# Kernel tuning notes

Measured on AMD Instinct MI355X. Metric: run time of the kernel, lower is better.

The kernel has to match this reference:

```python
import jax, jax.numpy as jnp
import numpy as np

B, L, D, H = 4, 1024, 1024, 16
DH = D // H


def setup_inputs() -> dict:
    key = jax.random.key(0)
    ks = jax.random.split(key, 10)
    x_embed = jax.random.normal(ks[0], (B, L, D), dtype=jnp.float32)
    bemb = jax.random.normal(ks[1], (B, L), dtype=jnp.float32)
    s = 0.02
    Wq_w = jax.random.normal(ks[2], (D, D), dtype=jnp.float32) * s
    Wk_w = jax.random.normal(ks[3], (D, D), dtype=jnp.float32) * s
    Wv_w = jax.random.normal(ks[4], (D, D), dtype=jnp.float32) * s
    Wo_w = jax.random.normal(ks[5], (D, D), dtype=jnp.float32) * s
    Wq_b = jnp.zeros((D,), jnp.float32)
    Wk_b = jnp.zeros((D,), jnp.float32)
    Wv_b = jnp.zeros((D,), jnp.float32)
    Wo_b = jnp.zeros((D,), jnp.float32)
    return dict(x_embed=x_embed, bemb=bemb, Wq_w=Wq_w, Wq_b=Wq_b,
                Wk_w=Wk_w, Wk_b=Wk_b, Wv_w=Wv_w, Wv_b=Wv_b,
                Wo_w=Wo_w, Wo_b=Wo_b)


def reference(x_embed, bemb, Wq_w, Wq_b, Wk_w, Wk_b, Wv_w, Wv_b, Wo_w, Wo_b):
    # present[b, l] = token l of batch b participates in attention
    present = bemb > 0  # [B, L]

    def proj(w, b):
        # torch Linear: y = x W^T + b; split heads -> [B, H, L, DH]
        y = jnp.einsum('bld,ed->ble', x_embed, w) + b
        return y.reshape(B, L, H, DH).transpose(0, 2, 1, 3)

    Q = proj(Wq_w, Wq_b)
    K = proj(Wk_w, Wk_b)
    V = proj(Wv_w, Wv_b)

    scores = jnp.einsum('bhqd,bhkd->bhqk', Q, K) / jnp.sqrt(jnp.float32(DH))
    # pre-softmax column mask: absent keys -> -inf
    scores = jnp.where(present[:, None, None, :], scores, -jnp.inf)
    A = jax.nn.softmax(scores, axis=-1)  # [B, H, L, L]
    # post-softmax row mask: subtract 1 on absent query rows, then relu
    row_absent = (~present).astype(A.dtype)[:, None, :, None]  # [B,1,L,1]
    A = jnp.maximum(A - row_absent, 0.0)

    out = jnp.einsum('bhqk,bhkd->bhqd', A, V)
    out = out.transpose(0, 2, 1, 3).reshape(B, L, D)
    out = jnp.einsum('bld,ed->ble', out, Wo_w) + Wo_b
    return out, A
```

## Files before the change

### kernel.cpp

```cpp
#include <hip/hip_runtime.h>
#include <math.h>

#define BB 4
#define LL 1024
#define DD 1024
#define HH 16
#define MROWS 4096

typedef __attribute__((ext_vector_type(8))) short short8;
typedef __attribute__((ext_vector_type(4))) float f32x4;
typedef __attribute__((ext_vector_type(4))) unsigned short us4;

__device__ inline unsigned short f2bf(float f) {
    unsigned int u = __builtin_bit_cast(unsigned int, f);
    u += 0x7fffu + ((u >> 16) & 1u);
    return (unsigned short)(u >> 16);
}

__device__ inline void gl2lds16(const void* g, void* l) {
    __builtin_amdgcn_global_load_lds(
        (const __attribute__((address_space(1))) void*)g,
        (__attribute__((address_space(3))) void*)l, 16, 0, 0);
}

__global__ __launch_bounds__(256) void cvt_all(const float* __restrict__ x,
                                               const float* __restrict__ wq,
                                               const float* __restrict__ wk,
                                               const float* __restrict__ wv,
                                               const float* __restrict__ wo,
                                               unsigned short* __restrict__ xb,
                                               unsigned short* __restrict__ wqb,
                                               unsigned short* __restrict__ wkb,
                                               unsigned short* __restrict__ wvb,
                                               unsigned short* __restrict__ wob) {
    int i = blockIdx.x * 256 + threadIdx.x;
    const float* src; unsigned short* dst; int k;
    if (i < 1048576) { src = x; dst = xb; k = i; }
    else {
        int j = i - 1048576; int w = j >> 18; k = j & 262143;
        src = (w == 0) ? wq : (w == 1) ? wk : (w == 2) ? wv : wo;
        dst = (w == 0) ? wqb : (w == 1) ? wkb : (w == 2) ? wvb : wob;
    }
    float4 v = ((const float4*)src)[k];
    us4 p = { f2bf(v.x), f2bf(v.y), f2bf(v.z), f2bf(v.w) };
    ((us4*)dst)[k] = p;
}

template<int BM>
__device__ __forceinline__ void gemm_core(const unsigned short* __restrict__ X,
                                          const unsigned short* __restrict__ W,
                                          const float* __restrict__ bias,
                                          void* __restrict__ Cv, int out_mode) {
    constexpr int MI = BM / 32;
    __shared__ unsigned short SMEM[(BM + 128) * 64];
    auto Xs = (unsigned short(*)[64])SMEM;
    auto Ws = (unsigned short(*)[64])(SMEM + BM * 64);
    const int t = threadIdx.x;
    const int lane = t & 63, quad = lane >> 4, lm = lane & 15;
    const int wave = t >> 6;
    const int mo = (wave & 1) * (BM / 2), no = (wave >> 1) * 64;
    const int row0 = blockIdx.x * BM, col0 = blockIdx.y * 128;
    const int sw = lm & 7;

    const int r_in = lane >> 3;
    const int sg = (lane & 7) ^ r_in;
    const unsigned short* xp = X + (size_t)(row0 + wave * (BM / 4) + r_in) * 1024 + sg * 8;
    const unsigned short* wp = W + (size_t)(col0 + wave * 32 + r_in) * 1024 + sg * 8;
    unsigned short* ldsX = &Xs[wave * (BM / 4)][0];
    unsigned short* ldsW = &Ws[wave * 32][0];

    f32x4 acc[MI][4] = {};

    for (int kc = 0; kc < 1024; kc += 64) {
        #pragma unroll
        for (int j = 0; j < BM / 32; ++j)
            gl2lds16(xp + (size_t)j * 8192 + kc, ldsX + j * 512);
        #pragma unroll
        for (int j = 0; j < 4; ++j)
            gl2lds16(wp + (size_t)j * 8192 + kc, ldsW + j * 512);
        __syncthreads();
        #pragma unroll
        for (int s = 0; s < 2; ++s) {
            short8 af[MI], bf[4];
            #pragma unroll
            for (int mi = 0; mi < MI; ++mi)
                af[mi] = *(const short8*)&Xs[mo + mi * 16 + lm][((s * 4 + quad) ^ sw) * 8];
            #pragma unroll
            for (int nj = 0; nj < 4; ++nj)
                bf[nj] = *(const short8*)&Ws[no + nj * 16 + lm][((s * 4 + quad) ^ sw) * 8];
            #pragma unroll
            for (int mi = 0; mi < MI; ++mi)
                #pragma unroll
                for (int nj = 0; nj < 4; ++nj)
                    acc[mi][nj] = __builtin_amdgcn_mfma_f32_16x16x32_bf16(
                        af[mi], bf[nj], acc[mi][nj], 0, 0, 0);
        }
        __syncthreads();
    }

    if constexpr (BM == 128) {
        if (out_mode == 2) {
            unsigned short* Ct = &SMEM[0];
            #pragma unroll
            for (int mi = 0; mi < 4; ++mi) {
                #pragma unroll
                for (int nj = 0; nj < 4; ++nj) {
                    int ccol = no + nj * 16 + lm;
                    int crow0 = mo + mi * 16 + quad * 4;
                    float bv = bias[col0 + ccol];
                    us4 pk = { f2bf(acc[mi][nj][0] + bv), f2bf(acc[mi][nj][1] + bv),
                               f2bf(acc[mi][nj][2] + bv), f2bf(acc[mi][nj][3] + bv) };
                    *(us4*)&Ct[ccol * 128 + (crow0 ^ ((ccol & 15) << 3))] = pk;
                }
            }
            __syncthreads();
            const int b = row0 >> 10, l0c = row0 & 1023;
            #pragma unroll
            for (int it = 0; it < 8; ++it) {
                int cc = (t >> 4) + it * 16;
                int lb = (t & 15) * 8;
                short8 v = *(const short8*)&Ct[cc * 128 + (lb ^ ((cc & 15) << 3))];
                int gcol = col0 + cc;
                int hh = gcol >> 6, dd = gcol & 63;
                *(short8*)&((unsigned short*)Cv)[(((size_t)b * 16 + hh) * 64 + dd) * 1024 + l0c + lb] = v;
            }
            return;
        }
    }

    #pragma unroll
    for (int mi = 0; mi < MI; ++mi) {
        #pragma unroll
        for (int nj = 0; nj < 4; ++nj) {
            int gr0 = row0 + mo + mi * 16 + quad * 4;
            int gc  = col0 + no + nj * 16 + lm;
            float bv = bias[gc];
            #pragma unroll
            for (int r = 0; r < 4; ++r) {
                float val = acc[mi][nj][r] + bv;
                int gr = gr0 + r;
                if (out_mode == 0) {
                    ((float*)Cv)[(size_t)gr * 1024 + gc] = val;
                } else {
                    ((unsigned short*)Cv)[(size_t)gr * 1024 + gc] = f2bf(val);
                }
            }
        }
    }
}

__global__ __launch_bounds__(256) void qkv_proj(const unsigned short* __restrict__ xb,
                                                const unsigned short* __restrict__ wq,
                                                const unsigned short* __restrict__ wk,
                                                const unsigned short* __restrict__ wv,
                                                const float* __restrict__ bq,
                                                const float* __restrict__ bk,
                                                const float* __restrict__ bv,
                                                unsigned short* __restrict__ Qw,
                                                unsigned short* __restrict__ Kw,
                                                unsigned short* __restrict__ Vt) {
    const int z = blockIdx.z;
    const unsigned short* W = (z == 0) ? wq : (z == 1) ? wk : wv;
    const float* b = (z == 0) ? bq : (z == 1) ? bk : bv;
    void* C = (z == 0) ? (void*)Qw : (z == 1) ? (void*)Kw : (void*)Vt;
    gemm_core<128>(xb, W, b, C, (z == 2) ? 2 : 1);
}

__global__ __launch_bounds__(256) void out_proj(const unsigned short* __restrict__ Aw,
                                                const unsigned short* __restrict__ wo,
                                                const float* __restrict__ bo,
                                                float* __restrict__ out) {
    gemm_core<64>(Aw, wo, bo, out, 0);
}

__global__ __launch_bounds__(512) void attn_fused(const unsigned short* __restrict__ Qw,
                                                  const unsigned short* __restrict__ Kw,
                                                  const unsigned short* __restrict__ Vt,
                                                  const float* __restrict__ bemb,
                                                  float* __restrict__ Aout,
                                                  unsigned short* __restrict__ attn) {
    __shared__ unsigned short Ks[128][64];
    __shared__ unsigned short Vs[64][128];
    __shared__ unsigned short Ps[8][16][66];
    __shared__ float maskadd[1024];
    const int t = threadIdx.x;
    const int lane = t & 63, quad = lane >> 4, lm = lane & 15;
    const int w = t >> 6;
    const int bh = blockIdx.x;
    const int q0 = blockIdx.y * 128;
    const int b = bh >> 4, h = bh & 15;
    const int qrow_frag = q0 + w * 16 + lm;
    const int qrow_acc0 = q0 + w * 16 + quad * 4;
    const int swk = lm & 7;

    const int kr_in = lane >> 3;
    const int ksg = (lane & 7) ^ kr_in;
    const unsigned short* kp = Kw + (size_t)(b * 1024 + w * 16 + kr_in) * 1024 + h * 64 + ksg * 8;
    unsigned short* ldsK = &Ks[w * 16][0];
    const int vr_in = lane >> 4, vcg = lane & 15;
    const int vrow = w * 8 + vr_in;
    const unsigned short* vpbase = Vt + (size_t)bh * 64 * 1024;
    unsigned short* ldsV = &Vs[w * 8][0];

    for (int i = t; i < 1024; i += 512)
        maskadd[i] = (bemb[b * 1024 + i] > 0.f) ? 0.f : -1e30f;

    short8 afq[2];
    #pragma unroll
    for (int s = 0; s < 2; ++s)
        afq[s] = *(const short8*)&Qw[(size_t)(b * 1024 + qrow_frag) * 1024 +
                                     h * 64 + s * 32 + quad * 8];

    float lsum[4] = { 0.f, 0.f, 0.f, 0.f };

    __syncthreads();

    for (int c = 0; c < 8; ++c) {
        #pragma unroll
        for (int j = 0; j < 2; ++j)
            gl2lds16(kp + (size_t)(c * 128 + j * 8) * 1024, ldsK + j * 512);
        __syncthreads();

        f32x4 acc[8] = {};
        #pragma unroll
        for (int s = 0; s < 2; ++s)
            #pragma unroll
            for (int nj = 0; nj < 8; ++nj) {
                short8 bfk = *(const short8*)&Ks[nj * 16 + lm][((s * 4 + quad) ^ swk) * 8];
                acc[nj] = __builtin_amdgcn_mfma_f32_16x16x32_bf16(afq[s], bfk, acc[nj], 0, 0, 0);
            }

        #pragma unroll
        for (int nj = 0; nj < 8; ++nj) {
            float ma = maskadd[c * 128 + nj * 16 + lm];
            #pragma unroll
            for (int r = 0; r < 4; ++r)
                lsum[r] += __expf(acc[nj][r] * 0.125f + ma);
        }
        __syncthreads();
    }

    float fnorm[4];
    #pragma unroll
    for (int r = 0; r < 4; ++r) {
        float s = lsum[r];
        #pragma unroll
        for (int off = 8; off >= 1; off >>= 1)
            s += __shfl_xor(s, off, 64);
        bool qp = bemb[b * 1024 + qrow_acc0 + r] > 0.f;
        fnorm[r] = (qp && s > 0.f) ? (1.f / s) : 0.f;
    }

    f32x4 oacc[4] = {};
    for (int c = 0; c < 8; ++c) {
        #pragma unroll
        for (int j = 0; j < 2; ++j) {
            gl2lds16(kp + (size_t)(c * 128 + j * 8) * 1024, ldsK + j * 512);
            int rl = vrow + j * 4;
            int vsg = vcg ^ (rl & 15);
            gl2lds16(vpbase + (size_t)rl * 1024 + c * 128 + vsg * 8, ldsV + j * 512);
        }
        __syncthreads();

        f32x4 acc[8] = {};
        #pragma unroll
        for (int s = 0; s < 2; ++s)
            #pragma unroll
            for (int nj = 0; nj < 8; ++nj) {
                short8 bfk = *(const short8*)&Ks[nj * 16 + lm][((s * 4 + quad) ^ swk) * 8];
                acc[nj] = __builtin_amdgcn_mfma_f32_16x16x32_bf16(afq[s], bfk, acc[nj], 0, 0, 0);
            }

        #pragma unroll
        for (int half = 0; half < 2; ++half) {
            #pragma unroll
            for (int nj4 = 0; nj4 < 4; ++nj4) {
                int nj = half * 4 + nj4;
                float ma = maskadd[c * 128 + nj * 16 + lm];
                #pragma unroll
                for (int r = 0; r < 4; ++r) {
                    float p  = __expf(acc[nj][r] * 0.125f + ma);
                    float a  = p * fnorm[r];
                    Aout[((size_t)bh * 1024 + qrow_acc0 + r) * 1024 + c * 128 + nj * 16 + lm] = a;
                    Ps[w][quad * 4 + r][nj4 * 16 + lm] = f2bf(a);
                }
            }
            #pragma unroll
            for (int ks2 = 0; ks2 < 2; ++ks2) {
                int ks = half * 2 + ks2;
                short8 afp = *(const short8*)&Ps[w][lm][ks2 * 32 + quad * 8];
                #pragma unroll
                for (int nd = 0; nd < 4; ++nd) {
                    short8 bfv = *(const short8*)&Vs[nd * 16 + lm][((ks * 4 + quad) ^ lm) * 8];
                    oacc[nd] = __builtin_amdgcn_mfma_f32_16x16x32_bf16(afp, bfv, oacc[nd], 0, 0, 0);
                }
            }
        }
        __syncthreads();
    }

    #pragma unroll
    for (int nd = 0; nd < 4; ++nd)
        #pragma unroll
        for (int r = 0; r < 4; ++r)
            attn[(size_t)(b * 1024 + qrow_acc0 + r) * 1024 + h * 64 + nd * 16 + lm] =
                f2bf(oacc[nd][r]);
}

extern "C" void kernel_launch(void* const* d_in, const int* in_sizes, int n_in,
                              void* d_out, int out_size, void* d_ws, size_t ws_size,
                              hipStream_t stream) {
    const float* x    = (const float*)d_in[0];
    const float* bemb = (const float*)d_in[1];
    const float* Wq   = (const float*)d_in[2];
    const float* Wq_b = (const float*)d_in[3];
    const float* Wk   = (const float*)d_in[4];
    const float* Wk_b = (const float*)d_in[5];
    const float* Wv   = (const float*)d_in[6];
    const float* Wv_b = (const float*)d_in[7];
    const float* Wo   = (const float*)d_in[8];
    const float* Wo_b = (const float*)d_in[9];

    float* out  = (float*)d_out;
    float* Aout = out + (size_t)BB * LL * DD;

    unsigned short* x_bf  = (unsigned short*)d_ws;
    unsigned short* Wq_bf = x_bf  + (size_t)MROWS * DD;
    unsigned short* Wk_bf = Wq_bf + (size_t)DD * DD;
    unsigned short* Wv_bf = Wk_bf + (size_t)DD * DD;
    unsigned short* Wo_bf = Wv_bf + (size_t)DD * DD;
    unsigned short* Qw    = Wo_bf + (size_t)DD * DD;
    unsigned short* Kw    = Qw + (size_t)MROWS * DD;
    unsigned short* Vt    = Kw + (size_t)MROWS * DD;
    unsigned short* Aw    = x_bf;

    cvt_all<<<dim3(8192), dim3(256), 0, stream>>>(x, Wq, Wk, Wv, Wo,
                                                  x_bf, Wq_bf, Wk_bf, Wv_bf, Wo_bf);

    qkv_proj<<<dim3(MROWS / 128, DD / 128, 3), dim3(256), 0, stream>>>(
        x_bf, Wq_bf, Wk_bf, Wv_bf, Wq_b, Wk_b, Wv_b, Qw, Kw, Vt);

    attn_fused<<<dim3(BB * HH, LL / 128), dim3(512), 0, stream>>>(
        Qw, Kw, Vt, bemb, Aout, Aw);

    out_proj<<<dim3(MROWS / 64, DD / 128), dim3(256), 0, stream>>>(
        Aw, Wo_bf, Wo_b, out);
}
```

Baseline: 415.8 us.

## Split attention softmax-denominator pass into separate higher-parallelism kernel

Moves the first pass that computes softmax row sums out of the fused attention kernel into its own kernel. The new kernel uses 64-row query tiles with 256 threads, giving more blocks, and writes the row sums to a global workspace. The second kernel reads those sums and performs normalisation, the A output and the PV product. This is meant to improve GPU occupancy for the sum pass. It adds a launch and a global round trip for the sums, and the QK^T work is still computed twice.

```diff
diff --git a/kernel.cpp b/kernel.cpp
--- a/kernel.cpp
+++ b/kernel.cpp
@@ -173,10 +173,81 @@
     gemm_core<64>(Aw, wo, bo, out, 0);
 }
 
-__global__ __launch_bounds__(512) void attn_fused(const unsigned short* __restrict__ Qw,
+__global__ __launch_bounds__(256) void attn_pass1(const unsigned short* __restrict__ Qw,
+                                                  const unsigned short* __restrict__ Kw,
+                                                  const float* __restrict__ bemb,
+                                                  float* __restrict__ Ls) {
+    __shared__ unsigned short Ks[128][64];
+    __shared__ float maskadd[1024];
+    const int t = threadIdx.x;
+    const int lane = t & 63, quad = lane >> 4, lm = lane & 15;
+    const int w = t >> 6;
+    const int bh = blockIdx.x;
+    const int q0 = blockIdx.y * 64;
+    const int b = bh >> 4, h = bh & 15;
+    const int qrow_frag = q0 + w * 16 + lm;
+    const int qrow_acc0 = q0 + w * 16 + quad * 4;
+    const int swk = lm & 7;
+
+    const int kr_in = lane >> 3;
+    const int ksg = (lane & 7) ^ kr_in;
+    const unsigned short* kp = Kw + (size_t)(b * 1024 + w * 32 + kr_in) * 1024 + h * 64 + ksg * 8;
+    unsigned short* ldsK = &Ks[w * 32][0];
+
+    for (int i = t; i < 1024; i += 256)
+        maskadd[i] = (bemb[b * 1024 + i] > 0.f) ? 0.f : -1e30f;
+
+    short8 afq[2];
+    #pragma unroll
+    for (int s = 0; s < 2; ++s)
+        afq[s] = *(const short8*)&Qw[(size_t)(b * 1024 + qrow_frag) * 1024 +
+                                     h * 64 + s * 32 + quad * 8];
+
+    float lsum[4] = { 0.f, 0.f, 0.f, 0.f };
+
+    __syncthreads();
+
+    for (int c = 0; c < 8; ++c) {
+        #pragma unroll
+        for (int j = 0; j < 4; ++j)
+            gl2lds16(kp + (size_t)(c * 128 + j * 8) * 1024, ldsK + j * 512);
+        __syncthreads();
+
+        f32x4 acc[8] = {};
+        #pragma unroll
+        for (int s = 0; s < 2; ++s)
+            #pragma unroll
+            for (int nj = 0; nj < 8; ++nj) {
+                short8 bfk = *(const short8*)&Ks[nj * 16 + lm][((s * 4 + quad) ^ swk) * 8];
+                acc[nj] = __builtin_amdgcn_mfma_f32_16x16x32_bf16(afq[s], bfk, acc[nj], 0, 0, 0);
+            }
+
+        #pragma unroll
+        for (int nj = 0; nj < 8; ++nj) {
+            float ma = maskadd[c * 128 + nj * 16 + lm];
+            #pragma unroll
+            for (int r = 0; r < 4; ++r)
+                lsum[r] += __expf(acc[nj][r] * 0.125f + ma);
+        }
+        __syncthreads();
+    }
+
+    #pragma unroll
+    for (int r = 0; r < 4; ++r) {
+        float s = lsum[r];
+        #pragma unroll
+        for (int off = 8; off >= 1; off >>= 1)
+            s += __shfl_xor(s, off, 64);
+        if (lm == r)
+            Ls[(size_t)bh * 1024 + qrow_acc0 + r] = s;
+    }
+}
+
+__global__ __launch_bounds__(512) void attn_pass2(const unsigned short* __restrict__ Qw,
                                                   const unsigned short* __restrict__ Kw,
                                                   const unsigned short* __restrict__ Vt,
                                                   const float* __restrict__ bemb,
+                                                  const float* __restrict__ Ls,
                                                   float* __restrict__ Aout,
                                                   unsigned short* __restrict__ attn) {
     __shared__ unsigned short Ks[128][64];
@@ -211,45 +282,15 @@
         afq[s] = *(const short8*)&Qw[(size_t)(b * 1024 + qrow_frag) * 1024 +
                                      h * 64 + s * 32 + quad * 8];
 
-    float lsum[4] = { 0.f, 0.f, 0.f, 0.f };
-
-    __syncthreads();
-
-    for (int c = 0; c < 8; ++c) {
-        #pragma unroll
-        for (int j = 0; j < 2; ++j)
-            gl2lds16(kp + (size_t)(c * 128 + j * 8) * 1024, ldsK + j * 512);
-        __syncthreads();
-
-        f32x4 acc[8] = {};
-        #pragma unroll
-        for (int s = 0; s < 2; ++s)
-            #pragma unroll
-            for (int nj = 0; nj < 8; ++nj) {
-                short8 bfk = *(const short8*)&Ks[nj * 16 + lm][((s * 4 + quad) ^ swk) * 8];
-                acc[nj] = __builtin_amdgcn_mfma_f32_16x16x32_bf16(afq[s], bfk, acc[nj], 0, 0, 0);
-            }
-
-        #pragma unroll
-        for (int nj = 0; nj < 8; ++nj) {
-            float ma = maskadd[c * 128 + nj * 16 + lm];
-            #pragma unroll
-            for (int r = 0; r < 4; ++r)
-                lsum[r] += __expf(acc[nj][r] * 0.125f + ma);
-        }
-        __syncthreads();
-    }
-
     float fnorm[4];
     #pragma unroll
     for (int r = 0; r < 4; ++r) {
-        float s = lsum[r];
-        #pragma unroll
-        for (int off = 8; off >= 1; off >>= 1)
-            s += __shfl_xor(s, off, 64);
+        float s = Ls[(size_t)bh * 1024 + qrow_acc0 + r];
         bool qp = bemb[b * 1024 + qrow_acc0 + r] > 0.f;
         fnorm[r] = (qp && s > 0.f) ? (1.f / s) : 0.f;
     }
+
+    __syncthreads();
 
     f32x4 oacc[4] = {};
     for (int c = 0; c < 8; ++c) {
@@ -332,6 +373,7 @@
     unsigned short* Qw    = Wo_bf + (size_t)DD * DD;
     unsigned short* Kw    = Qw + (size_t)MROWS * DD;
     unsigned short* Vt    = Kw + (size_t)MROWS * DD;
+    float*          Ls    = (float*)(Vt + (size_t)MROWS * DD);
     unsigned short* Aw    = x_bf;
 
     cvt_all<<<dim3(8192), dim3(256), 0, stream>>>(x, Wq, Wk, Wv, Wo,
@@ -340,8 +382,11 @@
     qkv_proj<<<dim3(MROWS / 128, DD / 128, 3), dim3(256), 0, stream>>>(
         x_bf, Wq_bf, Wk_bf, Wv_bf, Wq_b, Wk_b, Wv_b, Qw, Kw, Vt);
 
-    attn_fused<<<dim3(BB * HH, LL / 128), dim3(512), 0, stream>>>(
-        Qw, Kw, Vt, bemb, Aout, Aw);
+    attn_pass1<<<dim3(BB * HH, LL / 64), dim3(256), 0, stream>>>(
+        Qw, Kw, bemb, Ls);
+
+    attn_pass2<<<dim3(BB * HH, LL / 128), dim3(512), 0, stream>>>(
+        Qw, Kw, Vt, bemb, Ls, Aout, Aw);
 
     out_proj<<<dim3(MROWS / 64, DD / 128), dim3(256), 0, stream>>>(
         Aw, Wo_bf, Wo_b, out);
```

Measured after the change: 425.2 us. +2.3%, slower.
